# Kernel optimization log

Hardware: AMD Instinct MI355X
Metric: run time of the kernel (lower is better)

## Reference

```python
import jax, jax.numpy as jnp
import numpy as np

B, H, D = 16, 16, 128          # batch (decode seqs), heads, head_dim
BLK = 16                        # paged-KV block size (hard-coded in source)
MAXB = 128                      # blocks per sequence
MAXS = MAXB * BLK               # 2048 max context
NBLK = B * MAXB                 # total cache blocks
SOFTMAX_SCALE = 1.0 / np.sqrt(D)


def setup_inputs() -> dict:
    key = jax.random.key(0)
    ks = jax.random.split(key, 8)
    Q = jax.random.normal(ks[0], (B, H, D), dtype=jnp.float32)
    K = jax.random.normal(ks[1], (B, H, D), dtype=jnp.float32)
    V = jax.random.normal(ks[2], (B, H, D), dtype=jnp.float32)
    Kcache = jax.random.normal(ks[3], (NBLK, BLK, H, D), dtype=jnp.float32)
    Vcache = jax.random.normal(ks[4], (NBLK, BLK, H, D), dtype=jnp.float32)
    # context length per sequence (includes the new decode token)
    input_length = jax.random.randint(ks[5], (B,), 1, MAXS + 1).astype(jnp.int32)
    # each sequence owns a contiguous run of blocks
    block_tables = jnp.arange(B * MAXB, dtype=jnp.int32).reshape(B, MAXB)
    # flat slot index where the new token's K/V are written
    pos = input_length - 1
    save_slots = (block_tables[jnp.arange(B), pos // BLK] * BLK + pos % BLK).astype(jnp.int64)
    # per-token RoPE cos/sin
    ang = jax.random.uniform(ks[6], (B, D), dtype=jnp.float32) * (2.0 * np.pi)
    cos, sin = jnp.cos(ang), jnp.sin(ang)
    mask = jnp.zeros((B, MAXS), dtype=jnp.float32)  # additive attention bias
    return {"Q": Q, "K": K, "V": V, "Kcache": Kcache, "Vcache": Vcache,
            "cos": cos, "sin": sin, "mask": mask,
            "input_length": input_length, "save_slots": save_slots,
            "block_tables": block_tables, "max_s": MAXS}


def _rope(x, cos, sin):
    # LLaMA rotate-half RoPE; cos/sin are [B,1,D], x is [B,H,D]
    d2 = x.shape[-1] // 2
    x1, x2 = x[..., :d2], x[..., d2:]
    rot = jnp.concatenate([-x2, x1], axis=-1)
    return x * cos + rot * sin


def reference(Q, K, V, Kcache, Vcache, cos, sin, mask,
              input_length, save_slots, block_tables, max_s):
    c = cos[:, None, :]
    s = sin[:, None, :]
    qr = _rope(Q, c, s)                      # [B,H,D]
    kr = _rope(K, c, s)                      # [B,H,D]
    # scatter new token K/V into the paged cache (flat slot view)
    Kf = Kcache.reshape(-1, H, D).at[save_slots].set(kr)
    Vf = Vcache.reshape(-1, H, D).at[save_slots].set(V)
    # gather each sequence's context slots via its block table
    slot_idx = (block_tables[:, :, None] * BLK
                + jnp.arange(BLK, dtype=jnp.int32)).reshape(B, MAXS)  # [B,S]
    keys = Kf[slot_idx]                      # [B,S,H,D]
    vals = Vf[slot_idx]                      # [B,S,H,D]
    scores = jnp.einsum('bhd,bshd->bhs', qr, keys) * SOFTMAX_SCALE + mask[:, None, :]
    valid = jnp.arange(MAXS, dtype=jnp.int32)[None, :] < input_length[:, None]
    scores = jnp.where(valid[:, None, :], scores, jnp.float32(-1e30))
    p = jax.nn.softmax(scores, axis=-1)
    out = jnp.einsum('bhs,bshd->bhd', p, vals)  # [B,H,D]
    return out
```

## Files before the change

### kernel.cpp

```cpp
#include <hip/hip_runtime.h>

#define BATCH 16
#define NHEAD 16
#define DHEAD 128
#define BLK   16
#define MAXB  128
#define MAXS  (MAXB * BLK)
#define NSPLIT 8
#define CHUNK  (MAXS / NSPLIT)
#define SCALE  0.0883883476483184f

#define WSQ_FLOATS (BATCH * NHEAD * DHEAD)
#define PART_STRIDE (DHEAD + 2)

__global__ void rope_qk(const float* __restrict__ Q,
                        const float* __restrict__ K,
                        const float* __restrict__ cosb,
                        const float* __restrict__ sinb,
                        float* __restrict__ ws_q,
                        float* __restrict__ ws_k) {
    const int bh = blockIdx.x;
    const int b  = bh / NHEAD;
    const int d  = threadIdx.x;

    const float c = cosb[b * DHEAD + d];
    const float s = sinb[b * DHEAD + d];

    const size_t idx = (size_t)bh * DHEAD + d;
    const float qv = Q[idx];
    const float qrot = (d < DHEAD / 2) ? -Q[idx + DHEAD / 2] : Q[idx - DHEAD / 2];
    ws_q[idx] = qv * c + qrot * s;

    const float kv = K[idx];
    const float krot = (d < DHEAD / 2) ? -K[idx + DHEAD / 2] : K[idx - DHEAD / 2];
    ws_k[idx] = kv * c + krot * s;
}

__global__ __launch_bounds__(256) void attn_partial(
        const float* __restrict__ Kcache,
        const float* __restrict__ Vcache,
        const float* __restrict__ Vnew,
        const float* __restrict__ mask,
        const int* __restrict__ input_length,
        const int* __restrict__ block_tables,
        const float* __restrict__ ws_q,
        const float* __restrict__ ws_k,
        float* __restrict__ ws_part) {
    const int split = blockIdx.x;
    const int h     = blockIdx.y;
    const int b     = blockIdx.z;
    const int tid   = threadIdx.x;
    const int hw    = tid >> 5;
    const int ln    = tid & 31;

    __shared__ int   sbase[CHUNK];
    __shared__ float sp[CHUNK];
    __shared__ float sred[8];
    __shared__ float sacc[8][DHEAD];

    float* part = ws_part + ((size_t)((b * NHEAD + h) * NSPLIT + split)) * PART_STRIDE;

    const int L  = input_length[b];
    const int s0 = split * CHUNK;
    if (s0 >= L) {
        if (tid < DHEAD) part[tid] = 0.0f;
        if (tid == 0) { part[DHEAD] = -1e30f; part[DHEAD + 1] = 0.0f; }
        return;
    }
    const int n    = min(CHUNK, L - s0);
    const int iNew = (L - 1) - s0;

    const size_t bhoff = (size_t)(b * NHEAD + h) * DHEAD;

    if (tid < n) {
        const int s = s0 + tid;
        sbase[tid] = block_tables[b * MAXB + (s >> 4)] * (BLK * NHEAD * DHEAD)
                   + (s & (BLK - 1)) * (NHEAD * DHEAD) + h * DHEAD;
    }
    const float4 q = ((const float4*)(ws_q + bhoff))[ln];
    __syncthreads();

    #pragma unroll 4
    for (int i = hw; i < n; i += 8) {
        const float4 k = (i == iNew)
            ? ((const float4*)(ws_k + bhoff))[ln]
            : ((const float4*)(Kcache + sbase[i]))[ln];
        float d = k.x * q.x + k.y * q.y + k.z * q.z + k.w * q.w;
        #pragma unroll
        for (int off = 16; off >= 1; off >>= 1)
            d += __shfl_xor(d, off, 64);
        if (ln == 0) sp[i] = d;
    }
    __syncthreads();

    const float sc = (tid < n) ? sp[tid] * SCALE + mask[(size_t)b * MAXS + s0 + tid]
                               : -1e30f;
    float wm = sc;
    #pragma unroll
    for (int off = 32; off >= 1; off >>= 1)
        wm = fmaxf(wm, __shfl_xor(wm, off, 64));
    if ((tid & 63) == 0) sred[tid >> 6] = wm;
    __syncthreads();
    const float M = fmaxf(fmaxf(sred[0], sred[1]), fmaxf(sred[2], sred[3]));
    const float p = (tid < n) ? __expf(sc - M) : 0.0f;
    sp[tid] = p;
    float wsum = p;
    #pragma unroll
    for (int off = 32; off >= 1; off >>= 1)
        wsum += __shfl_xor(wsum, off, 64);
    if ((tid & 63) == 0) sred[4 + (tid >> 6)] = wsum;
    __syncthreads();
    const float l = (sred[4] + sred[5]) + (sred[6] + sred[7]);

    float4 acc = make_float4(0.0f, 0.0f, 0.0f, 0.0f);
    #pragma unroll 4
    for (int i = hw; i < n; i += 8) {
        const float4 v = (i == iNew)
            ? ((const float4*)(Vnew + bhoff))[ln]
            : ((const float4*)(Vcache + sbase[i]))[ln];
        const float pi = sp[i];
        acc.x += pi * v.x;
        acc.y += pi * v.y;
        acc.z += pi * v.z;
        acc.w += pi * v.w;
    }

    ((float4*)sacc[hw])[ln] = acc;
    __syncthreads();
    if (tid < DHEAD) {
        float a = 0.0f;
        #pragma unroll
        for (int w = 0; w < 8; ++w) a += sacc[w][tid];
        part[tid] = a;
        if (tid == 0) { part[DHEAD] = M; part[DHEAD + 1] = l; }
    }
}

__global__ void attn_combine(const float* __restrict__ ws_part,
                             float* __restrict__ out) {
    const int bh = blockIdx.x;
    const int d  = threadIdx.x;

    const float* base = ws_part + (size_t)bh * NSPLIT * PART_STRIDE;

    float M = -1e30f;
    #pragma unroll
    for (int s = 0; s < NSPLIT; ++s)
        M = fmaxf(M, base[s * PART_STRIDE + DHEAD]);

    float lsum = 0.0f, a = 0.0f;
    #pragma unroll
    for (int s = 0; s < NSPLIT; ++s) {
        const float f = __expf(base[s * PART_STRIDE + DHEAD] - M);
        lsum += base[s * PART_STRIDE + DHEAD + 1] * f;
        a    += base[s * PART_STRIDE + d] * f;
    }
    out[(size_t)bh * DHEAD + d] = a / lsum;
}

extern "C" void kernel_launch(void* const* d_in, const int* in_sizes, int n_in,
                              void* d_out, int out_size, void* d_ws, size_t ws_size,
                              hipStream_t stream) {
    const float* Q       = (const float*)d_in[0];
    const float* K       = (const float*)d_in[1];
    const float* V       = (const float*)d_in[2];
    const float* Kcache  = (const float*)d_in[3];
    const float* Vcache  = (const float*)d_in[4];
    const float* cosb    = (const float*)d_in[5];
    const float* sinb    = (const float*)d_in[6];
    const float* mask    = (const float*)d_in[7];
    const int*   in_len  = (const int*)d_in[8];
    const int*   btab    = (const int*)d_in[10];

    float* ws_q    = (float*)d_ws;
    float* ws_k    = ws_q + WSQ_FLOATS;
    float* ws_part = ws_k + WSQ_FLOATS;
    float* out     = (float*)d_out;

    rope_qk<<<BATCH * NHEAD, DHEAD, 0, stream>>>(Q, K, cosb, sinb, ws_q, ws_k);

    dim3 grid2(NSPLIT, NHEAD, BATCH);
    attn_partial<<<grid2, 256, 0, stream>>>(
        Kcache, Vcache, V, mask, in_len, btab, ws_q, ws_k, ws_part);

    attn_combine<<<BATCH * NHEAD, DHEAD, 0, stream>>>(ws_part, out);
}
```

Before: 482.5 us.

## Fuse RoPE into attention kernel and use single-pass online softmax

Removes the separate RoPE launch by computing rotated Q (pre-scaled) and the new K inside each attention block via shared memory. The two passes over K and V are merged into one loop with a per-half-warp online softmax, with the per-warp partials combined by rescaling at the end. K and V cache loads are issued together, so more memory traffic is in flight and one launch is saved. In exchange each block redundantly recomputes RoPE, and the loop does two extra exponentials per row.

```diff
diff --git a/kernel.cpp b/kernel.cpp
--- a/kernel.cpp
+++ b/kernel.cpp
@@ -10,41 +10,19 @@
 #define CHUNK  (MAXS / NSPLIT)
 #define SCALE  0.0883883476483184f
 
-#define WSQ_FLOATS (BATCH * NHEAD * DHEAD)
 #define PART_STRIDE (DHEAD + 2)
 
-__global__ void rope_qk(const float* __restrict__ Q,
-                        const float* __restrict__ K,
-                        const float* __restrict__ cosb,
-                        const float* __restrict__ sinb,
-                        float* __restrict__ ws_q,
-                        float* __restrict__ ws_k) {
-    const int bh = blockIdx.x;
-    const int b  = bh / NHEAD;
-    const int d  = threadIdx.x;
-
-    const float c = cosb[b * DHEAD + d];
-    const float s = sinb[b * DHEAD + d];
-
-    const size_t idx = (size_t)bh * DHEAD + d;
-    const float qv = Q[idx];
-    const float qrot = (d < DHEAD / 2) ? -Q[idx + DHEAD / 2] : Q[idx - DHEAD / 2];
-    ws_q[idx] = qv * c + qrot * s;
-
-    const float kv = K[idx];
-    const float krot = (d < DHEAD / 2) ? -K[idx + DHEAD / 2] : K[idx - DHEAD / 2];
-    ws_k[idx] = kv * c + krot * s;
-}
-
 __global__ __launch_bounds__(256) void attn_partial(
+        const float* __restrict__ Q,
+        const float* __restrict__ K,
+        const float* __restrict__ V,
         const float* __restrict__ Kcache,
         const float* __restrict__ Vcache,
-        const float* __restrict__ Vnew,
+        const float* __restrict__ cosb,
+        const float* __restrict__ sinb,
         const float* __restrict__ mask,
         const int* __restrict__ input_length,
         const int* __restrict__ block_tables,
-        const float* __restrict__ ws_q,
-        const float* __restrict__ ws_k,
         float* __restrict__ ws_part) {
     const int split = blockIdx.x;
     const int h     = blockIdx.y;
@@ -54,8 +32,10 @@
     const int ln    = tid & 31;
 
     __shared__ int   sbase[CHUNK];
-    __shared__ float sp[CHUNK];
-    __shared__ float sred[8];
+    __shared__ float smask[CHUNK];
+    __shared__ float sq[DHEAD];
+    __shared__ float sknew[DHEAD];
+    __shared__ float sred[16];
     __shared__ float sacc[8][DHEAD];
 
     float* part = ws_part + ((size_t)((b * NHEAD + h) * NSPLIT + split)) * PART_STRIDE;
@@ -76,63 +56,66 @@
         const int s = s0 + tid;
         sbase[tid] = block_tables[b * MAXB + (s >> 4)] * (BLK * NHEAD * DHEAD)
                    + (s & (BLK - 1)) * (NHEAD * DHEAD) + h * DHEAD;
+        smask[tid] = mask[(size_t)b * MAXS + s];
     }
-    const float4 q = ((const float4*)(ws_q + bhoff))[ln];
+    if (tid < DHEAD) {
+        const float c  = cosb[b * DHEAD + tid];
+        const float sn = sinb[b * DHEAD + tid];
+        const float qv = Q[bhoff + tid];
+        const float qr = (tid < DHEAD / 2) ? -Q[bhoff + tid + DHEAD / 2]
+                                           :  Q[bhoff + tid - DHEAD / 2];
+        sq[tid] = (qv * c + qr * sn) * SCALE;
+        const float kv = K[bhoff + tid];
+        const float kr = (tid < DHEAD / 2) ? -K[bhoff + tid + DHEAD / 2]
+                                           :  K[bhoff + tid - DHEAD / 2];
+        sknew[tid] = kv * c + kr * sn;
+    }
     __syncthreads();
 
-    #pragma unroll 4
+    const float4 q    = ((const float4*)sq)[ln];
+    const float4 knew = ((const float4*)sknew)[ln];
+
+    float  m = -1e30f, l = 0.0f;
+    float4 acc = make_float4(0.0f, 0.0f, 0.0f, 0.0f);
+    #pragma unroll 2
     for (int i = hw; i < n; i += 8) {
-        const float4 k = (i == iNew)
-            ? ((const float4*)(ws_k + bhoff))[ln]
-            : ((const float4*)(Kcache + sbase[i]))[ln];
+        const int base = sbase[i];
+        const float4 k = (i == iNew) ? knew
+                                     : ((const float4*)(Kcache + base))[ln];
+        const float4 v = (i == iNew) ? ((const float4*)(V + bhoff))[ln]
+                                     : ((const float4*)(Vcache + base))[ln];
         float d = k.x * q.x + k.y * q.y + k.z * q.z + k.w * q.w;
         #pragma unroll
         for (int off = 16; off >= 1; off >>= 1)
             d += __shfl_xor(d, off, 64);
-        if (ln == 0) sp[i] = d;
-    }
-    __syncthreads();
-
-    const float sc = (tid < n) ? sp[tid] * SCALE + mask[(size_t)b * MAXS + s0 + tid]
-                               : -1e30f;
-    float wm = sc;
-    #pragma unroll
-    for (int off = 32; off >= 1; off >>= 1)
-        wm = fmaxf(wm, __shfl_xor(wm, off, 64));
-    if ((tid & 63) == 0) sred[tid >> 6] = wm;
-    __syncthreads();
-    const float M = fmaxf(fmaxf(sred[0], sred[1]), fmaxf(sred[2], sred[3]));
-    const float p = (tid < n) ? __expf(sc - M) : 0.0f;
-    sp[tid] = p;
-    float wsum = p;
-    #pragma unroll
-    for (int off = 32; off >= 1; off >>= 1)
-        wsum += __shfl_xor(wsum, off, 64);
-    if ((tid & 63) == 0) sred[4 + (tid >> 6)] = wsum;
-    __syncthreads();
-    const float l = (sred[4] + sred[5]) + (sred[6] + sred[7]);
-
-    float4 acc = make_float4(0.0f, 0.0f, 0.0f, 0.0f);
-    #pragma unroll 4
-    for (int i = hw; i < n; i += 8) {
-        const float4 v = (i == iNew)
-            ? ((const float4*)(Vnew + bhoff))[ln]
-            : ((const float4*)(Vcache + sbase[i]))[ln];
-        const float pi = sp[i];
-        acc.x += pi * v.x;
-        acc.y += pi * v.y;
-        acc.z += pi * v.z;
-        acc.w += pi * v.w;
+        d += smask[i];
+        const float mn = fmaxf(m, d);
+        const float r  = __expf(m - mn);
+        const float p  = __expf(d - mn);
+        l = l * r + p;
+        acc.x = acc.x * r + p * v.x;
+        acc.y = acc.y * r + p * v.y;
+        acc.z = acc.z * r + p * v.z;
+        acc.w = acc.w * r + p * v.w;
+        m = mn;
     }
 
+    if (ln == 0) { sred[hw] = m; sred[8 + hw] = l; }
     ((float4*)sacc[hw])[ln] = acc;
     __syncthreads();
     if (tid < DHEAD) {
-        float a = 0.0f;
+        float M = sred[0];
         #pragma unroll
-        for (int w = 0; w < 8; ++w) a += sacc[w][tid];
+        for (int w = 1; w < 8; ++w) M = fmaxf(M, sred[w]);
+        float lsum = 0.0f, a = 0.0f;
+        #pragma unroll
+        for (int w = 0; w < 8; ++w) {
+            const float f = __expf(sred[w] - M);
+            lsum += sred[8 + w] * f;
+            a    += sacc[w][tid] * f;
+        }
         part[tid] = a;
-        if (tid == 0) { part[DHEAD] = M; part[DHEAD + 1] = l; }
+        if (tid == 0) { part[DHEAD] = M; part[DHEAD + 1] = lsum; }
     }
 }
 
@@ -172,16 +155,12 @@
     const int*   in_len  = (const int*)d_in[8];
     const int*   btab    = (const int*)d_in[10];
 
-    float* ws_q    = (float*)d_ws;
-    float* ws_k    = ws_q + WSQ_FLOATS;
-    float* ws_part = ws_k + WSQ_FLOATS;
+    float* ws_part = (float*)d_ws;
     float* out     = (float*)d_out;
 
-    rope_qk<<<BATCH * NHEAD, DHEAD, 0, stream>>>(Q, K, cosb, sinb, ws_q, ws_k);
-
-    dim3 grid2(NSPLIT, NHEAD, BATCH);
-    attn_partial<<<grid2, 256, 0, stream>>>(
-        Kcache, Vcache, V, mask, in_len, btab, ws_q, ws_k, ws_part);
+    dim3 grid(NSPLIT, NHEAD, BATCH);
+    attn_partial<<<grid, 256, 0, stream>>>(
+        Q, K, V, Kcache, Vcache, cosb, sinb, mask, in_len, btab, ws_part);
 
     attn_combine<<<BATCH * NHEAD, DHEAD, 0, stream>>>(ws_part, out);
 }
```

New measurement: 500.5 us. 1.04x slower.
